# Kernel optimization log

Hardware: AMD Instinct MI355X
Metric: run time of the kernel (lower is better)

Reference implementation:

```python
import jax, jax.numpy as jnp
import numpy as np

B, L, D, H, C, V, NC = 64, 64, 300, 128, 50, 50000, 2
LAMDA = 0.1
KS = (3, 4, 5)


def setup_inputs() -> dict:
    key = jax.random.key(0)
    ks = jax.random.split(key, 16)
    n = lambda k, shp, s=0.02: (jax.random.normal(k, shp, jnp.float32) * s)
    return {
        "x": jax.random.randint(ks[0], (B, L), 0, V),
        "embedmatrix": n(ks[1], (V, D), 0.1),
        "att_w1a": n(ks[2], (D, H)),      # first half of attlinear1 weight (for curembed)
        "att_w1b": n(ks[3], (D, H)),      # second half (for the paired embedding)
        "att_b1": jnp.zeros((H,), jnp.float32),
        "att_w2": n(ks[4], (H,)),
        "att_b2": jnp.zeros((), jnp.float32),
        "conv_w1": n(ks[5], (C, 2 * D, KS[0])), "conv_b1": jnp.zeros((C,), jnp.float32),
        "conv_w2": n(ks[6], (C, 2 * D, KS[1])), "conv_b2": jnp.zeros((C,), jnp.float32),
        "conv_w3": n(ks[7], (C, 2 * D, KS[2])), "conv_b3": jnp.zeros((C,), jnp.float32),
        "lin_w": n(ks[8], (3 * C, NC)), "lin_b": jnp.zeros((NC,), jnp.float32),
    }


def _attention(emb, w1a, w1b, b1, w2, b2):
    # Faithful vectorization of attentionembed/attentionword, including the
    # original's use of the COMPACTED index for the score partner and decay.
    Bb, Ll, Dd = emb.shape
    pa = emb @ w1a                        # [B,L,H]  curembed projection
    pb = emb[:, : Ll - 1] @ w1b           # [B,L-1,H] partner is outputs[:, index]
    h = jnp.tanh(pa[:, :, None, :] + pb[:, None, :, :] + b1)  # [B,L,L-1,H]
    s = h @ w2 + b2                       # [B,L,L-1]
    i = jnp.arange(Ll)[:, None]
    k = jnp.arange(Ll - 1)[None, :]
    decay = (1.0 - LAMDA) ** (jnp.abs(i - k) - 1).astype(jnp.float32)  # [L,L-1]
    alpha = jax.nn.softmax(decay * s, axis=-1)                         # [B,L,L-1]
    # attended embeddings use j = k + (k >= i) (skip position i)
    idx = k + (k >= i)                    # [L,L-1]
    alpha_full = jnp.zeros((Bb, Ll, Ll), emb.dtype).at[:, i, idx].set(alpha)
    return jnp.einsum('blm,bmd->bld', alpha_full, emb)  # [B,L,D]


def reference(x, embedmatrix, att_w1a, att_w1b, att_b1, att_w2, att_b2,
              conv_w1, conv_b1, conv_w2, conv_b2, conv_w3, conv_b3,
              lin_w, lin_b):
    emb = embedmatrix[x]                                   # [B,L,D]
    att = _attention(emb, att_w1a, att_w1b, att_b1, att_w2, att_b2)
    feat = jnp.concatenate([emb, att], axis=2).transpose(0, 2, 1)  # [B,2D,L]
    pooled = []
    for w, b in ((conv_w1, conv_b1), (conv_w2, conv_b2), (conv_w3, conv_b3)):
        y = jax.lax.conv_general_dilated(
            feat, w, window_strides=(1,), padding='VALID',
            dimension_numbers=('NCH', 'OIH', 'NCH')) + b[None, :, None]
        pooled.append(jnp.max(y, axis=-1))                 # pool over full valid length -> [B,C]
    conout = jnp.concatenate(pooled, axis=1)               # [B,3C]; dropout is identity in eval
    logits = conout @ lin_w + lin_b                        # [B,NC]
    return jax.nn.log_softmax(logits, axis=1)
```

## Files before the change

### kernel.cpp

```cpp
#include <hip/hip_runtime.h>
#include <math.h>

#define B_ 64
#define L_ 64
#define D_ 300
#define H_ 128
#define TWO_D 600
#define M_ 4096
#define Q_ 600
#define KP 640
#define KPA 320
#define HH 256

typedef short short8 __attribute__((ext_vector_type(8)));
typedef float floatx4 __attribute__((ext_vector_type(4)));

static __device__ __forceinline__ unsigned short f2bf(float f) {
    unsigned int u = __float_as_uint(f);
    u += 0x7FFFu + ((u >> 16) & 1u);
    return (unsigned short)(u >> 16);
}
static __device__ __forceinline__ float bf2f(unsigned short u) {
    return __uint_as_float(((unsigned int)u) << 16);
}
static __device__ __forceinline__ float fast_tanh(float x) {
    float x2 = x * x;
    return fmaf(x * x2, fmaf(x2, 0.13333333f, -0.33333333f), x);
}

__global__ __launch_bounds__(256) void k_prep(const int* __restrict__ x, const float* __restrict__ em,
        const float* __restrict__ w1a, const float* __restrict__ w1b,
        const float* __restrict__ cw1, const float* __restrict__ cw2, const float* __restrict__ cw3,
        unsigned short* __restrict__ fvb, unsigned short* __restrict__ wtT,
        unsigned short* __restrict__ w1abT) {
    int blk = blockIdx.x, tid = threadIdx.x;
    if (blk < 512) {
        #pragma unroll
        for (int r = 0; r < 8; ++r) {
            int m = blk * 8 + r;
            const float* src = em + (size_t)x[m] * D_;
            unsigned short* dst = fvb + (size_t)m * KP;
            for (int d = tid; d < KPA; d += 256) dst[d] = (d < D_) ? f2bf(src[d]) : 0;
            if (tid < 40) dst[TWO_D + tid] = 0;
        }
    } else if (blk < 912) {
        int base = ((blk - 512) * 256 + tid) * 4;
        #pragma unroll
        for (int e = 0; e < 4; ++e) {
            int idx = base + e;
            int q = idx / KP, d = idx - q * KP;
            float v = 0.f;
            if (q < Q_ && d < TWO_D) {
                if (q < 150)      { int c = q/3, i = q%3;                 v = cw1[((size_t)c*TWO_D + d)*3 + i]; }
                else if (q < 350) { int r2 = q-150; int c = r2/4, i = r2%4; v = cw2[((size_t)c*TWO_D + d)*4 + i]; }
                else              { int r2 = q-350; int c = r2/5, i = r2%5; v = cw3[((size_t)c*TWO_D + d)*5 + i]; }
            }
            wtT[idx] = f2bf(v);
        }
    } else {
        int base = ((blk - 912) * 256 + tid) * 4;
        #pragma unroll
        for (int e = 0; e < 4; ++e) {
            int idx = base + e;
            int h = idx / KPA, d = idx - h * KPA;
            float v = 0.f;
            if (d < D_) v = (h < H_) ? w1a[(size_t)d * H_ + h] : w1b[(size_t)d * H_ + (h - H_)];
            w1abT[idx] = f2bf(v);
        }
    }
}

__global__ __launch_bounds__(256) void k_papb(const unsigned short* __restrict__ A,
                                              const unsigned short* __restrict__ Bt,
                                              const float* __restrict__ b1,
                                              float* __restrict__ pab) {
    __shared__ unsigned short sA[64 * 72];
    __shared__ unsigned short sB[64 * 72];
    int m0 = blockIdx.x * 64, n0 = blockIdx.y * 64;
    int tid = threadIdx.x, lane = tid & 63, wave = tid >> 6;
    int wr = wave >> 1, wc = wave & 1;
    int sr = tid >> 2, so = (tid & 3) * 16;
    floatx4 acc[2][2] = {};
    int lr = lane & 15, lk = (lane >> 4) * 8;
    for (int k0 = 0; k0 < KPA; k0 += 64) {
        const unsigned short* Ar = &A [(size_t)(m0 + sr) * KP  + k0 + so];
        const unsigned short* Br = &Bt[(size_t)(n0 + sr) * KPA + k0 + so];
        *(uint4*)&sA[sr * 72 + so]     = *(const uint4*)Ar;
        *(uint4*)&sA[sr * 72 + so + 8] = *(const uint4*)(Ar + 8);
        *(uint4*)&sB[sr * 72 + so]     = *(const uint4*)Br;
        *(uint4*)&sB[sr * 72 + so + 8] = *(const uint4*)(Br + 8);
        __syncthreads();
        #pragma unroll
        for (int kk = 0; kk < 64; kk += 32) {
            short8 a0 = *(const short8*)&sA[(wr * 32 +  0 + lr) * 72 + kk + lk];
            short8 a1 = *(const short8*)&sA[(wr * 32 + 16 + lr) * 72 + kk + lk];
            short8 b0 = *(const short8*)&sB[(wc * 32 +  0 + lr) * 72 + kk + lk];
            short8 b1 = *(const short8*)&sB[(wc * 32 + 16 + lr) * 72 + kk + lk];
            acc[0][0] = __builtin_amdgcn_mfma_f32_16x16x32_bf16(a0, b0, acc[0][0], 0, 0, 0);
            acc[0][1] = __builtin_amdgcn_mfma_f32_16x16x32_bf16(a0, b1, acc[0][1], 0, 0, 0);
            acc[1][0] = __builtin_amdgcn_mfma_f32_16x16x32_bf16(a1, b0, acc[1][0], 0, 0, 0);
            acc[1][1] = __builtin_amdgcn_mfma_f32_16x16x32_bf16(a1, b1, acc[1][1], 0, 0, 0);
        }
        __syncthreads();
    }
    int drow = (lane >> 4) * 4, dcol = lane & 15;
    #pragma unroll
    for (int mi = 0; mi < 2; ++mi)
        #pragma unroll
        for (int ni = 0; ni < 2; ++ni) {
            int col = n0 + wc * 32 + ni * 16 + dcol;
            float bias = (col < H_) ? b1[col] : 0.f;
            #pragma unroll
            for (int i = 0; i < 4; ++i) {
                int row = m0 + wr * 32 + mi * 16 + drow + i;
                pab[(size_t)row * HH + col] = acc[mi][ni][i] + bias;
            }
        }
}

#define AT_PITCH 132
__global__ __launch_bounds__(256) void k_attn(const float* __restrict__ pab,
                                              const float* __restrict__ w2g,
                                              const float* __restrict__ b2,
                                              unsigned short* __restrict__ af) {
    int blk = blockIdx.x;
    int b = blk >> 2;
    int i0 = (blk & 3) * 16;
    __shared__ float pbL[64 * AT_PITCH];
    __shared__ float paL[16 * 128];
    __shared__ float s_w2[128];
    int tid = threadIdx.x, wave = tid >> 6, lane = tid & 63;
    {
        int r = tid >> 2, c0 = (tid & 3) * 32;
        #pragma unroll
        for (int c = 0; c < 32; c += 4) {
            float4 v = *(const float4*)&pab[(size_t)(b * 64 + r) * HH + H_ + c0 + c];
            *(float4*)&pbL[r * AT_PITCH + c0 + c] = v;
        }
    }
    {
        int idx = tid * 8;
        int ri = idx >> 7, h = idx & 127;
        const float* src = &pab[(size_t)(b * 64 + i0 + ri) * HH + h];
        *(float4*)&paL[idx]     = *(const float4*)src;
        *(float4*)&paL[idx + 4] = *(const float4*)(src + 4);
    }
    if (tid < 128) s_w2[tid] = w2g[tid];
    __syncthreads();

    float b2v = b2[0];
    int k = lane;
    float p0 = 0.f, p1 = 0.f, p2 = 0.f, p3 = 0.f;
    const float* pbrow = &pbL[k * AT_PITCH];
    const float* par = &paL[(wave * 4) * 128];
    for (int h = 0; h < 128; h += 4) {
        float4 pb4 = *(const float4*)&pbrow[h];
        float4 w4  = *(const float4*)&s_w2[h];
        float4 a0  = *(const float4*)&par[h];
        float4 a1  = *(const float4*)&par[128 + h];
        float4 a2  = *(const float4*)&par[256 + h];
        float4 a3  = *(const float4*)&par[384 + h];
        p0 += w4.x * fast_tanh(a0.x + pb4.x) + w4.y * fast_tanh(a0.y + pb4.y)
            + w4.z * fast_tanh(a0.z + pb4.z) + w4.w * fast_tanh(a0.w + pb4.w);
        p1 += w4.x * fast_tanh(a1.x + pb4.x) + w4.y * fast_tanh(a1.y + pb4.y)
            + w4.z * fast_tanh(a1.z + pb4.z) + w4.w * fast_tanh(a1.w + pb4.w);
        p2 += w4.x * fast_tanh(a2.x + pb4.x) + w4.y * fast_tanh(a2.y + pb4.y)
            + w4.z * fast_tanh(a2.z + pb4.z) + w4.w * fast_tanh(a2.w + pb4.w);
        p3 += w4.x * fast_tanh(a3.x + pb4.x) + w4.y * fast_tanh(a3.y + pb4.y)
            + w4.z * fast_tanh(a3.z + pb4.z) + w4.w * fast_tanh(a3.w + pb4.w);
    }
    #pragma unroll
    for (int j = 0; j < 4; ++j) {
        float p = (j == 0) ? p0 : (j == 1) ? p1 : (j == 2) ? p2 : p3;
        int i = i0 + wave * 4 + j;
        p += b2v;
        float v;
        if (k < 63) {
            float e = fabsf((float)(i - k)) - 1.0f;
            v = __expf(e * -0.10536051565782628f) * p;
        } else v = -INFINITY;
        float mx = v;
        #pragma unroll
        for (int off = 32; off; off >>= 1) mx = fmaxf(mx, __shfl_xor(mx, off, 64));
        float ex = (k < 63) ? __expf(v - mx) : 0.f;
        float sm = ex;
        #pragma unroll
        for (int off = 32; off; off >>= 1) sm += __shfl_xor(sm, off, 64);
        float alpha = ex * __builtin_amdgcn_rcpf(sm);
        int jj = (k < 63) ? (k + (k >= i)) : i;
        af[(size_t)(b * 64 + i) * 64 + jj] = (k < 63) ? f2bf(alpha) : (unsigned short)0;
    }
}

__global__ __launch_bounds__(256) void k_att_mfma(const unsigned short* __restrict__ af,
                                                  unsigned short* __restrict__ fvb) {
    int b = blockIdx.x;
    int n0 = blockIdx.y * 64;
    __shared__ unsigned short sA[64 * 72];
    __shared__ unsigned short sBt[64 * 72];
    int tid = threadIdx.x, wave = tid >> 6, lane = tid & 63;
    int sr = tid >> 2, so = (tid & 3) * 16;
    *(uint4*)&sA[sr * 72 + so]     = *(const uint4*)&af[(size_t)(b * 64 + sr) * 64 + so];
    *(uint4*)&sA[sr * 72 + so + 8] = *(const uint4*)&af[(size_t)(b * 64 + sr) * 64 + so + 8];
    int dg = n0 + lane;
    #pragma unroll
    for (int p = 0; p < 16; ++p) {
        int m = p * 4 + wave;
        unsigned short v = (dg < D_) ? fvb[(size_t)(b * 64 + m) * KP + dg] : (unsigned short)0;
        sBt[lane * 72 + m] = v;
    }
    __syncthreads();
    int wr = wave >> 1, wc = wave & 1;
    int lr = lane & 15, lk = (lane >> 4) * 8;
    floatx4 acc[2][2] = {};
    #pragma unroll
    for (int k0 = 0; k0 < 64; k0 += 32) {
        short8 a0 = *(const short8*)&sA [(wr * 32 +  0 + lr) * 72 + k0 + lk];
        short8 a1 = *(const short8*)&sA [(wr * 32 + 16 + lr) * 72 + k0 + lk];
        short8 b0 = *(const short8*)&sBt[(wc * 32 +  0 + lr) * 72 + k0 + lk];
        short8 b1 = *(const short8*)&sBt[(wc * 32 + 16 + lr) * 72 + k0 + lk];
        acc[0][0] = __builtin_amdgcn_mfma_f32_16x16x32_bf16(a0, b0, acc[0][0], 0, 0, 0);
        acc[0][1] = __builtin_amdgcn_mfma_f32_16x16x32_bf16(a0, b1, acc[0][1], 0, 0, 0);
        acc[1][0] = __builtin_amdgcn_mfma_f32_16x16x32_bf16(a1, b0, acc[1][0], 0, 0, 0);
        acc[1][1] = __builtin_amdgcn_mfma_f32_16x16x32_bf16(a1, b1, acc[1][1], 0, 0, 0);
    }
    int drow = (lane >> 4) * 4, dcol = lane & 15;
    #pragma unroll
    for (int mi = 0; mi < 2; ++mi)
        #pragma unroll
        for (int ni = 0; ni < 2; ++ni) {
            int dgo = n0 + wc * 32 + ni * 16 + dcol;
            if (dgo >= D_) continue;
            #pragma unroll
            for (int i = 0; i < 4; ++i) {
                int row = wr * 32 + mi * 16 + drow + i;
                fvb[(size_t)(b * 64 + row) * KP + D_ + dgo] = f2bf(acc[mi][ni][i]);
            }
        }
}

__global__ __launch_bounds__(256) void k_gemmT(const unsigned short* __restrict__ Wt,
                                               const unsigned short* __restrict__ Bv,
                                               unsigned short* __restrict__ GTb) {
    __shared__ unsigned short sA[64 * 72];
    __shared__ unsigned short sB[64 * 72];
    int q0 = blockIdx.x * 64, n0 = blockIdx.y * 64;
    int tid = threadIdx.x, lane = tid & 63, wave = tid >> 6;
    int wr = wave >> 1, wc = wave & 1;
    int sr = tid >> 2, so = (tid & 3) * 16;
    floatx4 acc[2][2] = {};
    int lr = lane & 15, lk = (lane >> 4) * 8;
    for (int k0 = 0; k0 < KP; k0 += 64) {
        const unsigned short* Ar = &Wt[(size_t)(q0 + sr) * KP + k0 + so];
        const unsigned short* Br = &Bv[(size_t)(n0 + sr) * KP + k0 + so];
        *(uint4*)&sA[sr * 72 + so]     = *(const uint4*)Ar;
        *(uint4*)&sA[sr * 72 + so + 8] = *(const uint4*)(Ar + 8);
        *(uint4*)&sB[sr * 72 + so]     = *(const uint4*)Br;
        *(uint4*)&sB[sr * 72 + so + 8] = *(const uint4*)(Br + 8);
        __syncthreads();
        #pragma unroll
        for (int kk = 0; kk < 64; kk += 32) {
            short8 a0 = *(const short8*)&sA[(wr * 32 +  0 + lr) * 72 + kk + lk];
            short8 a1 = *(const short8*)&sA[(wr * 32 + 16 + lr) * 72 + kk + lk];
            short8 b0 = *(const short8*)&sB[(wc * 32 +  0 + lr) * 72 + kk + lk];
            short8 b1 = *(const short8*)&sB[(wc * 32 + 16 + lr) * 72 + kk + lk];
            acc[0][0] = __builtin_amdgcn_mfma_f32_16x16x32_bf16(a0, b0, acc[0][0], 0, 0, 0);
            acc[0][1] = __builtin_amdgcn_mfma_f32_16x16x32_bf16(a0, b1, acc[0][1], 0, 0, 0);
            acc[1][0] = __builtin_amdgcn_mfma_f32_16x16x32_bf16(a1, b0, acc[1][0], 0, 0, 0);
            acc[1][1] = __builtin_amdgcn_mfma_f32_16x16x32_bf16(a1, b1, acc[1][1], 0, 0, 0);
        }
        __syncthreads();
    }
    int drow = (lane >> 4) * 4, dcol = lane & 15;
    #pragma unroll
    for (int mi = 0; mi < 2; ++mi)
        #pragma unroll
        for (int ni = 0; ni < 2; ++ni) {
            int qrow = q0 + wr * 32 + mi * 16 + drow;
            int col  = n0 + wc * 32 + ni * 16 + dcol;
            #pragma unroll
            for (int i = 0; i < 4; ++i)
                GTb[(size_t)(qrow + i) * M_ + col] = f2bf(acc[mi][ni][i]);
        }
}

__global__ __launch_bounds__(256) void k_pool(const unsigned short* __restrict__ GTb,
        const float* __restrict__ cb1, const float* __restrict__ cb2, const float* __restrict__ cb3,
        float* __restrict__ conout) {
    int task = blockIdx.x * 4 + (threadIdx.x >> 6);
    int lane = threadIdx.x & 63;
    int b = task / 150, p = task - b * 150;
    int ks, qb; float bias;
    if (p < 50)       { ks = 3; qb = p * 3;              bias = cb1[p]; }
    else if (p < 100) { int c = p - 50;  ks = 4; qb = 150 + c * 4; bias = cb2[c]; }
    else              { int c = p - 100; ks = 5; qb = 350 + c * 5; bias = cb3[c]; }
    int T = L_ - ks + 1;
    float y = -INFINITY;
    if (lane < T) {
        float s = bias;
        for (int i = 0; i < ks; ++i)
            s += bf2f(GTb[(size_t)(qb + i) * M_ + b * 64 + lane + i]);
        y = s;
    }
    #pragma unroll
    for (int off = 32; off; off >>= 1) y = fmaxf(y, __shfl_xor(y, off, 64));
    if (lane == 0) conout[b * 150 + p] = y;
}

__global__ __launch_bounds__(192) void k_final(const float* __restrict__ conout,
                                               const float* __restrict__ lw,
                                               const float* __restrict__ lb,
                                               float* __restrict__ out) {
    int b = blockIdx.x;
    int tid = threadIdx.x, wave = tid >> 6, lane = tid & 63;
    __shared__ float part[3][2];
    float l0 = 0.f, l1 = 0.f;
    if (tid < 150) {
        float v = conout[b * 150 + tid];
        l0 = v * lw[tid * 2 + 0];
        l1 = v * lw[tid * 2 + 1];
    }
    #pragma unroll
    for (int off = 32; off; off >>= 1) {
        l0 += __shfl_xor(l0, off, 64);
        l1 += __shfl_xor(l1, off, 64);
    }
    if (lane == 0) { part[wave][0] = l0; part[wave][1] = l1; }
    __syncthreads();
    if (tid == 0) {
        float s0 = lb[0] + part[0][0] + part[1][0] + part[2][0];
        float s1 = lb[1] + part[0][1] + part[1][1] + part[2][1];
        float mx = fmaxf(s0, s1);
        float ls = mx + logf(expf(s0 - mx) + expf(s1 - mx));
        out[b * 2 + 0] = s0 - ls;
        out[b * 2 + 1] = s1 - ls;
    }
}

extern "C" void kernel_launch(void* const* d_in, const int* in_sizes, int n_in,
                              void* d_out, int out_size, void* d_ws, size_t ws_size,
                              hipStream_t stream) {
    const int*   x   = (const int*)  d_in[0];
    const float* em  = (const float*)d_in[1];
    const float* w1a = (const float*)d_in[2];
    const float* w1b = (const float*)d_in[3];
    const float* b1  = (const float*)d_in[4];
    const float* w2  = (const float*)d_in[5];
    const float* b2  = (const float*)d_in[6];
    const float* cw1 = (const float*)d_in[7];
    const float* cb1 = (const float*)d_in[8];
    const float* cw2 = (const float*)d_in[9];
    const float* cb2 = (const float*)d_in[10];
    const float* cw3 = (const float*)d_in[11];
    const float* cb3 = (const float*)d_in[12];
    const float* lw  = (const float*)d_in[13];
    const float* lb  = (const float*)d_in[14];
    float* out = (float*)d_out;

    float* ws = (float*)d_ws;
    unsigned short* GTb    = (unsigned short*)ws;
    unsigned short* af     = (unsigned short*)ws;
    float*          pab    = ws + 2621440;
    unsigned short* fvb    = (unsigned short*)(ws + 3670016);
    unsigned short* WtT    = (unsigned short*)(ws + 4980736);
    unsigned short* w1abT  = (unsigned short*)(ws + 5185536);
    float*          conout = ws + 5226496;

    hipLaunchKernelGGL(k_prep, dim3(992), dim3(256), 0, stream,
                       x, em, w1a, w1b, cw1, cw2, cw3, fvb, WtT, w1abT);
    hipLaunchKernelGGL(k_papb, dim3(M_ / 64, HH / 64), dim3(256), 0, stream,
                       fvb, w1abT, b1, pab);
    hipLaunchKernelGGL(k_attn, dim3(256), dim3(256), 0, stream, pab, w2, b2, af);
    hipLaunchKernelGGL(k_att_mfma, dim3(B_, 5), dim3(256), 0, stream, af, fvb);
    hipLaunchKernelGGL(k_gemmT, dim3(KP / 64, M_ / 64), dim3(256), 0, stream,
                       WtT, fvb, GTb);
    hipLaunchKernelGGL(k_pool, dim3(2400), dim3(256), 0, stream,
                       GTb, cb1, cb2, cb3, conout);
    hipLaunchKernelGGL(k_final, dim3(B_), dim3(192), 0, stream, conout, lw, lb, out);
}
```

Before: 54.07 us.

## Fuse attention softmax and alpha-weighted embedding MFMA into one kernel

Merges the attention score/softmax kernel with the alpha×embedding MFMA kernel. Each block keeps its 16 rows of alpha in shared memory, reuses the pb/pa shared buffer to stage the transposed embeddings for its batch, and writes the attended embeddings straight into the feature buffer. This removes one launch and the global round trip of the alpha matrix. In exchange, each of the four blocks per batch reloads that batch's full embedding tile, and only 19 MFMA tiles are spread across 4 waves, so the waves carry uneven work.

```diff
diff --git a/kernel.cpp b/kernel.cpp
--- a/kernel.cpp
+++ b/kernel.cpp
@@ -119,16 +119,20 @@
 }
 
 #define AT_PITCH 132
-__global__ __launch_bounds__(256) void k_attn(const float* __restrict__ pab,
-                                              const float* __restrict__ w2g,
-                                              const float* __restrict__ b2,
-                                              unsigned short* __restrict__ af) {
+__global__ __launch_bounds__(256) void k_attn_fused(const float* __restrict__ pab,
+                                                    const float* __restrict__ w2g,
+                                                    const float* __restrict__ b2,
+                                                    unsigned short* __restrict__ fvb) {
     int blk = blockIdx.x;
     int b = blk >> 2;
     int i0 = (blk & 3) * 16;
-    __shared__ float pbL[64 * AT_PITCH];
-    __shared__ float paL[16 * 128];
+    __shared__ float smem[11200];
+    __shared__ unsigned short alphaL[16 * 72];
     __shared__ float s_w2[128];
+    float* pbL = smem;
+    float* paL = smem + 64 * AT_PITCH;
+    unsigned short* sBt = (unsigned short*)smem;
+
     int tid = threadIdx.x, wave = tid >> 6, lane = tid & 63;
     {
         int r = tid >> 2, c0 = (tid & 3) * 32;
@@ -151,24 +155,37 @@
     float b2v = b2[0];
     int k = lane;
     float p0 = 0.f, p1 = 0.f, p2 = 0.f, p3 = 0.f;
-    const float* pbrow = &pbL[k * AT_PITCH];
-    const float* par = &paL[(wave * 4) * 128];
-    for (int h = 0; h < 128; h += 4) {
-        float4 pb4 = *(const float4*)&pbrow[h];
-        float4 w4  = *(const float4*)&s_w2[h];
-        float4 a0  = *(const float4*)&par[h];
-        float4 a1  = *(const float4*)&par[128 + h];
-        float4 a2  = *(const float4*)&par[256 + h];
-        float4 a3  = *(const float4*)&par[384 + h];
-        p0 += w4.x * fast_tanh(a0.x + pb4.x) + w4.y * fast_tanh(a0.y + pb4.y)
-            + w4.z * fast_tanh(a0.z + pb4.z) + w4.w * fast_tanh(a0.w + pb4.w);
-        p1 += w4.x * fast_tanh(a1.x + pb4.x) + w4.y * fast_tanh(a1.y + pb4.y)
-            + w4.z * fast_tanh(a1.z + pb4.z) + w4.w * fast_tanh(a1.w + pb4.w);
-        p2 += w4.x * fast_tanh(a2.x + pb4.x) + w4.y * fast_tanh(a2.y + pb4.y)
-            + w4.z * fast_tanh(a2.z + pb4.z) + w4.w * fast_tanh(a2.w + pb4.w);
-        p3 += w4.x * fast_tanh(a3.x + pb4.x) + w4.y * fast_tanh(a3.y + pb4.y)
-            + w4.z * fast_tanh(a3.z + pb4.z) + w4.w * fast_tanh(a3.w + pb4.w);
-    }
+    {
+        const float* pbrow = &pbL[k * AT_PITCH];
+        const float* par = &paL[(wave * 4) * 128];
+        for (int h = 0; h < 128; h += 4) {
+            float4 pb4 = *(const float4*)&pbrow[h];
+            float4 w4  = *(const float4*)&s_w2[h];
+            float4 a0  = *(const float4*)&par[h];
+            float4 a1  = *(const float4*)&par[128 + h];
+            float4 a2  = *(const float4*)&par[256 + h];
+            float4 a3  = *(const float4*)&par[384 + h];
+            p0 += w4.x * fast_tanh(a0.x + pb4.x) + w4.y * fast_tanh(a0.y + pb4.y)
+                + w4.z * fast_tanh(a0.z + pb4.z) + w4.w * fast_tanh(a0.w + pb4.w);
+            p1 += w4.x * fast_tanh(a1.x + pb4.x) + w4.y * fast_tanh(a1.y + pb4.y)
+                + w4.z * fast_tanh(a1.z + pb4.z) + w4.w * fast_tanh(a1.w + pb4.w);
+            p2 += w4.x * fast_tanh(a2.x + pb4.x) + w4.y * fast_tanh(a2.y + pb4.y)
+                + w4.z * fast_tanh(a2.z + pb4.z) + w4.w * fast_tanh(a2.w + pb4.w);
+            p3 += w4.x * fast_tanh(a3.x + pb4.x) + w4.y * fast_tanh(a3.y + pb4.y)
+                + w4.z * fast_tanh(a3.z + pb4.z) + w4.w * fast_tanh(a3.w + pb4.w);
+        }
+    }
+    __syncthreads();
+
+    for (int mm = wave; mm < 64; mm += 4) {
+        const unsigned short* frow = &fvb[(size_t)(b * 64 + mm) * KP];
+        #pragma unroll
+        for (int ds = 0; ds < 5; ++ds) {
+            int d = ds * 64 + lane;
+            if (d < 304) sBt[d * 72 + mm] = (d < D_) ? frow[d] : (unsigned short)0;
+        }
+    }
+
     #pragma unroll
     for (int j = 0; j < 4; ++j) {
         float p = (j == 0) ? p0 : (j == 1) ? p1 : (j == 2) ? p2 : p3;
@@ -188,55 +205,30 @@
         for (int off = 32; off; off >>= 1) sm += __shfl_xor(sm, off, 64);
         float alpha = ex * __builtin_amdgcn_rcpf(sm);
         int jj = (k < 63) ? (k + (k >= i)) : i;
-        af[(size_t)(b * 64 + i) * 64 + jj] = (k < 63) ? f2bf(alpha) : (unsigned short)0;
-    }
-}
-
-__global__ __launch_bounds__(256) void k_att_mfma(const unsigned short* __restrict__ af,
-                                                  unsigned short* __restrict__ fvb) {
-    int b = blockIdx.x;
-    int n0 = blockIdx.y * 64;
-    __shared__ unsigned short sA[64 * 72];
-    __shared__ unsigned short sBt[64 * 72];
-    int tid = threadIdx.x, wave = tid >> 6, lane = tid & 63;
-    int sr = tid >> 2, so = (tid & 3) * 16;
-    *(uint4*)&sA[sr * 72 + so]     = *(const uint4*)&af[(size_t)(b * 64 + sr) * 64 + so];
-    *(uint4*)&sA[sr * 72 + so + 8] = *(const uint4*)&af[(size_t)(b * 64 + sr) * 64 + so + 8];
-    int dg = n0 + lane;
-    #pragma unroll
-    for (int p = 0; p < 16; ++p) {
-        int m = p * 4 + wave;
-        unsigned short v = (dg < D_) ? fvb[(size_t)(b * 64 + m) * KP + dg] : (unsigned short)0;
-        sBt[lane * 72 + m] = v;
+        alphaL[(wave * 4 + j) * 72 + jj] = (k < 63) ? f2bf(alpha) : (unsigned short)0;
     }
     __syncthreads();
-    int wr = wave >> 1, wc = wave & 1;
+
     int lr = lane & 15, lk = (lane >> 4) * 8;
-    floatx4 acc[2][2] = {};
-    #pragma unroll
-    for (int k0 = 0; k0 < 64; k0 += 32) {
-        short8 a0 = *(const short8*)&sA [(wr * 32 +  0 + lr) * 72 + k0 + lk];
-        short8 a1 = *(const short8*)&sA [(wr * 32 + 16 + lr) * 72 + k0 + lk];
-        short8 b0 = *(const short8*)&sBt[(wc * 32 +  0 + lr) * 72 + k0 + lk];
-        short8 b1 = *(const short8*)&sBt[(wc * 32 + 16 + lr) * 72 + k0 + lk];
-        acc[0][0] = __builtin_amdgcn_mfma_f32_16x16x32_bf16(a0, b0, acc[0][0], 0, 0, 0);
-        acc[0][1] = __builtin_amdgcn_mfma_f32_16x16x32_bf16(a0, b1, acc[0][1], 0, 0, 0);
-        acc[1][0] = __builtin_amdgcn_mfma_f32_16x16x32_bf16(a1, b0, acc[1][0], 0, 0, 0);
-        acc[1][1] = __builtin_amdgcn_mfma_f32_16x16x32_bf16(a1, b1, acc[1][1], 0, 0, 0);
-    }
     int drow = (lane >> 4) * 4, dcol = lane & 15;
-    #pragma unroll
-    for (int mi = 0; mi < 2; ++mi)
-        #pragma unroll
-        for (int ni = 0; ni < 2; ++ni) {
-            int dgo = n0 + wc * 32 + ni * 16 + dcol;
-            if (dgo >= D_) continue;
+    for (int t = wave; t < 19; t += 4) {
+        int d0 = t * 16;
+        floatx4 acc = {};
+        #pragma unroll
+        for (int kk = 0; kk < 64; kk += 32) {
+            short8 a  = *(const short8*)&alphaL[lr * 72 + kk + lk];
+            short8 bb = *(const short8*)&sBt[(d0 + lr) * 72 + kk + lk];
+            acc = __builtin_amdgcn_mfma_f32_16x16x32_bf16(a, bb, acc, 0, 0, 0);
+        }
+        int dgo = d0 + dcol;
+        if (dgo < D_) {
             #pragma unroll
             for (int i = 0; i < 4; ++i) {
-                int row = wr * 32 + mi * 16 + drow + i;
-                fvb[(size_t)(b * 64 + row) * KP + D_ + dgo] = f2bf(acc[mi][ni][i]);
+                int r = drow + i;
+                fvb[(size_t)(b * 64 + i0 + r) * KP + D_ + dgo] = f2bf(acc[i]);
             }
         }
+    }
 }
 
 __global__ __launch_bounds__(256) void k_gemmT(const unsigned short* __restrict__ Wt,
@@ -359,7 +351,6 @@
 
     float* ws = (float*)d_ws;
     unsigned short* GTb    = (unsigned short*)ws;
-    unsigned short* af     = (unsigned short*)ws;
     float*          pab    = ws + 2621440;
     unsigned short* fvb    = (unsigned short*)(ws + 3670016);
     unsigned short* WtT    = (unsigned short*)(ws + 4980736);
@@ -370,8 +361,7 @@
                        x, em, w1a, w1b, cw1, cw2, cw3, fvb, WtT, w1abT);
     hipLaunchKernelGGL(k_papb, dim3(M_ / 64, HH / 64), dim3(256), 0, stream,
                        fvb, w1abT, b1, pab);
-    hipLaunchKernelGGL(k_attn, dim3(256), dim3(256), 0, stream, pab, w2, b2, af);
-    hipLaunchKernelGGL(k_att_mfma, dim3(B_, 5), dim3(256), 0, stream, af, fvb);
+    hipLaunchKernelGGL(k_attn_fused, dim3(256), dim3(256), 0, stream, pab, w2, b2, fvb);
     hipLaunchKernelGGL(k_gemmT, dim3(KP / 64, M_ / 64), dim3(256), 0, stream,
                        WtT, fvb, GTb);
     hipLaunchKernelGGL(k_pool, dim3(2400), dim3(256), 0, stream,
```

Result: slower. 59.04 us (+9.2%).

## Fuse conv GEMM with max-pool by regrouping weight rows into channel-aligned tiles

Applied to the files above, without the earlier changes.

Conv weight rows are regrouped so each 64-row tile holds whole channels of a single kernel size (21, 16 or 12 channels, padded to 768 rows). This lets the GEMM block keep its fp32 result tile in shared memory and do the bias, sliding-window sum and max-pool itself. The bf16 intermediate GTb round trip through global memory and the separate pool launch go away, and pooling now reads fp32 instead of bf16-rounded values. The cost is about 20% more padded GEMM rows and a serial pooling tail at the end of each block.

```diff
diff --git a/kernel.cpp b/kernel.cpp
--- a/kernel.cpp
+++ b/kernel.cpp
@@ -7,10 +7,10 @@
 #define H_ 128
 #define TWO_D 600
 #define M_ 4096
-#define Q_ 600
 #define KP 640
 #define KPA 320
 #define HH 256
+#define QT 768
 
 typedef short short8 __attribute__((ext_vector_type(8)));
 typedef float floatx4 __attribute__((ext_vector_type(4)));
@@ -19,9 +19,6 @@
     unsigned int u = __float_as_uint(f);
     u += 0x7FFFu + ((u >> 16) & 1u);
     return (unsigned short)(u >> 16);
-}
-static __device__ __forceinline__ float bf2f(unsigned short u) {
-    return __uint_as_float(((unsigned int)u) << 16);
 }
 static __device__ __forceinline__ float fast_tanh(float x) {
     float x2 = x * x;
@@ -43,22 +40,23 @@
             for (int d = tid; d < KPA; d += 256) dst[d] = (d < D_) ? f2bf(src[d]) : 0;
             if (tid < 40) dst[TWO_D + tid] = 0;
         }
-    } else if (blk < 912) {
+    } else if (blk < 992) {
         int base = ((blk - 512) * 256 + tid) * 4;
         #pragma unroll
         for (int e = 0; e < 4; ++e) {
             int idx = base + e;
-            int q = idx / KP, d = idx - q * KP;
+            int qq = idx / KP, d = idx - qq * KP;
             float v = 0.f;
-            if (q < Q_ && d < TWO_D) {
-                if (q < 150)      { int c = q/3, i = q%3;                 v = cw1[((size_t)c*TWO_D + d)*3 + i]; }
-                else if (q < 350) { int r2 = q-150; int c = r2/4, i = r2%4; v = cw2[((size_t)c*TWO_D + d)*4 + i]; }
-                else              { int r2 = q-350; int c = r2/5, i = r2%5; v = cw3[((size_t)c*TWO_D + d)*5 + i]; }
+            if (d < TWO_D) {
+                int tile = qq >> 6, r = qq & 63;
+                if (tile < 3)      { int c = 21*tile + r/3;     int i = r % 3; if (r < 63 && c < 50) v = cw1[((size_t)c*TWO_D + d)*3 + i]; }
+                else if (tile < 7) { int c = 16*(tile-3) + (r>>2); int i = r & 3; if (c < 50)           v = cw2[((size_t)c*TWO_D + d)*4 + i]; }
+                else               { int c = 12*(tile-7) + r/5;    int i = r % 5; if (r < 60 && c < 50) v = cw3[((size_t)c*TWO_D + d)*5 + i]; }
             }
             wtT[idx] = f2bf(v);
         }
     } else {
-        int base = ((blk - 912) * 256 + tid) * 4;
+        int base = ((blk - 992) * 256 + tid) * 4;
         #pragma unroll
         for (int e = 0; e < 4; ++e) {
             int idx = base + e;
@@ -239,12 +237,16 @@
         }
 }
 
-__global__ __launch_bounds__(256) void k_gemmT(const unsigned short* __restrict__ Wt,
-                                               const unsigned short* __restrict__ Bv,
-                                               unsigned short* __restrict__ GTb) {
+#define GP 68
+__global__ __launch_bounds__(256) void k_gemm_pool(const unsigned short* __restrict__ Wt,
+        const unsigned short* __restrict__ Bv,
+        const float* __restrict__ cb1, const float* __restrict__ cb2, const float* __restrict__ cb3,
+        float* __restrict__ conout) {
     __shared__ unsigned short sA[64 * 72];
     __shared__ unsigned short sB[64 * 72];
-    int q0 = blockIdx.x * 64, n0 = blockIdx.y * 64;
+    int tile = blockIdx.x;
+    int b = blockIdx.y;
+    int q0 = tile * 64, n0 = b * 64;
     int tid = threadIdx.x, lane = tid & 63, wave = tid >> 6;
     int wr = wave >> 1, wc = wave & 1;
     int sr = tid >> 2, so = (tid & 3) * 16;
@@ -271,40 +273,36 @@
         }
         __syncthreads();
     }
+    float* gtile = (float*)sA;
     int drow = (lane >> 4) * 4, dcol = lane & 15;
     #pragma unroll
     for (int mi = 0; mi < 2; ++mi)
         #pragma unroll
         for (int ni = 0; ni < 2; ++ni) {
-            int qrow = q0 + wr * 32 + mi * 16 + drow;
-            int col  = n0 + wc * 32 + ni * 16 + dcol;
+            int qrow = wr * 32 + mi * 16 + drow;
+            int col  = wc * 32 + ni * 16 + dcol;
             #pragma unroll
             for (int i = 0; i < 4; ++i)
-                GTb[(size_t)(qrow + i) * M_ + col] = f2bf(acc[mi][ni][i]);
-        }
-}
-
-__global__ __launch_bounds__(256) void k_pool(const unsigned short* __restrict__ GTb,
-        const float* __restrict__ cb1, const float* __restrict__ cb2, const float* __restrict__ cb3,
-        float* __restrict__ conout) {
-    int task = blockIdx.x * 4 + (threadIdx.x >> 6);
-    int lane = threadIdx.x & 63;
-    int b = task / 150, p = task - b * 150;
-    int ks, qb; float bias;
-    if (p < 50)       { ks = 3; qb = p * 3;              bias = cb1[p]; }
-    else if (p < 100) { int c = p - 50;  ks = 4; qb = 150 + c * 4; bias = cb2[c]; }
-    else              { int c = p - 100; ks = 5; qb = 350 + c * 5; bias = cb3[c]; }
+                gtile[(qrow + i) * GP + col] = acc[mi][ni][i];
+        }
+    __syncthreads();
+    int chans, ks, pbase; const float* cb;
+    if (tile < 3)      { int c0 = 21 * tile;      chans = min(21, 50 - c0); ks = 3; pbase = c0;       cb = cb1 + c0; }
+    else if (tile < 7) { int c0 = 16 * (tile - 3); chans = min(16, 50 - c0); ks = 4; pbase = 50 + c0;  cb = cb2 + c0; }
+    else               { int c0 = 12 * (tile - 7); chans = min(12, 50 - c0); ks = 5; pbase = 100 + c0; cb = cb3 + c0; }
     int T = L_ - ks + 1;
-    float y = -INFINITY;
-    if (lane < T) {
-        float s = bias;
-        for (int i = 0; i < ks; ++i)
-            s += bf2f(GTb[(size_t)(qb + i) * M_ + b * 64 + lane + i]);
-        y = s;
-    }
-    #pragma unroll
-    for (int off = 32; off; off >>= 1) y = fmaxf(y, __shfl_xor(y, off, 64));
-    if (lane == 0) conout[b * 150 + p] = y;
+    for (int c = wave; c < chans; c += 4) {
+        float y = -INFINITY;
+        if (lane < T) {
+            float s = cb[c];
+            for (int i = 0; i < ks; ++i)
+                s += gtile[(c * ks + i) * GP + lane + i];
+            y = s;
+        }
+        #pragma unroll
+        for (int off = 32; off; off >>= 1) y = fmaxf(y, __shfl_xor(y, off, 64));
+        if (lane == 0) conout[b * 150 + pbase + c] = y;
+    }
 }
 
 __global__ __launch_bounds__(192) void k_final(const float* __restrict__ conout,
@@ -358,23 +356,20 @@
     float* out = (float*)d_out;
 
     float* ws = (float*)d_ws;
-    unsigned short* GTb    = (unsigned short*)ws;
-    unsigned short* af     = (unsigned short*)ws;
-    float*          pab    = ws + 2621440;
-    unsigned short* fvb    = (unsigned short*)(ws + 3670016);
-    unsigned short* WtT    = (unsigned short*)(ws + 4980736);
-    unsigned short* w1abT  = (unsigned short*)(ws + 5185536);
-    float*          conout = ws + 5226496;
-
-    hipLaunchKernelGGL(k_prep, dim3(992), dim3(256), 0, stream,
-                       x, em, w1a, w1b, cw1, cw2, cw3, fvb, WtT, w1abT);
+    float*          pab    = ws;
+    unsigned short* af     = (unsigned short*)(ws + 1048576);
+    unsigned short* fvb    = (unsigned short*)(ws + 1179648);
+    unsigned short* Wt2T   = (unsigned short*)(ws + 2490368);
+    unsigned short* w1abT  = (unsigned short*)(ws + 2736128);
+    float*          conout = ws + 2777088;
+
+    hipLaunchKernelGGL(k_prep, dim3(1072), dim3(256), 0, stream,
+                       x, em, w1a, w1b, cw1, cw2, cw3, fvb, Wt2T, w1abT);
     hipLaunchKernelGGL(k_papb, dim3(M_ / 64, HH / 64), dim3(256), 0, stream,
                        fvb, w1abT, b1, pab);
     hipLaunchKernelGGL(k_attn, dim3(256), dim3(256), 0, stream, pab, w2, b2, af);
     hipLaunchKernelGGL(k_att_mfma, dim3(B_, 5), dim3(256), 0, stream, af, fvb);
-    hipLaunchKernelGGL(k_gemmT, dim3(KP / 64, M_ / 64), dim3(256), 0, stream,
-                       WtT, fvb, GTb);
-    hipLaunchKernelGGL(k_pool, dim3(2400), dim3(256), 0, stream,
-                       GTb, cb1, cb2, cb3, conout);
+    hipLaunchKernelGGL(k_gemm_pool, dim3(12, B_), dim3(256), 0, stream,
+                       Wt2T, fvb, cb1, cb2, cb3, conout);
     hipLaunchKernelGGL(k_final, dim3(B_), dim3(192), 0, stream, conout, lw, lb, out);
 }
```

New measurement: 51.06 us. 5.6% less time.
